# Kernel optimization log

Measured on AMD Instinct MI355X. Metric: run time of the kernel, lower is better.

Reference implementation:

```python
import jax, jax.numpy as jnp
import numpy as np

N, D, H, L = 100000, 128, 4, 2
C = D // H  # per-head channels
E = 1600000
NEG_SLOPE = 0.2
LN_EPS = 1e-5


def setup_inputs() -> dict:
    key = jax.random.key(0)
    ks = jax.random.split(key, 8)
    x = jax.random.normal(ks[0], (N, D), dtype=jnp.float32)
    edge_index = jax.random.randint(ks[1], (2, E), 0, N, dtype=jnp.int64)
    s = 1.0 / np.sqrt(D)
    Wl = jax.random.normal(ks[2], (L, D, D), dtype=jnp.float32) * s
    Wr = jax.random.normal(ks[3], (L, D, D), dtype=jnp.float32) * s
    att = jax.random.normal(ks[4], (L, H, C), dtype=jnp.float32) * (1.0 / np.sqrt(C))
    bias = jnp.zeros((L, D), dtype=jnp.float32)
    gamma = jnp.ones((L, D), dtype=jnp.float32)
    beta = jnp.zeros((L, D), dtype=jnp.float32)
    return {"x": x, "edge_index": edge_index, "Wl": Wl, "Wr": Wr,
            "att": att, "bias": bias, "gamma": gamma, "beta": beta}


def _gatv2_layer(h, src, dst, Wl, Wr, att, bias):
    # h: (N, D); src/dst: (E2,) with self-loops already appended
    xl = (h @ Wl).reshape(N, H, C)  # source-side transform
    xr = (h @ Wr).reshape(N, H, C)  # target-side transform
    e = jax.nn.leaky_relu(xl[src] + xr[dst], NEG_SLOPE)      # (E2, H, C)
    alpha = jnp.einsum('ehc,hc->eh', e, att)                 # (E2, H)
    # segment softmax over incoming edges of each destination node
    m = jax.ops.segment_max(alpha, dst, num_segments=N)      # (N, H)
    ea = jnp.exp(alpha - m[dst])
    s = jax.ops.segment_sum(ea, dst, num_segments=N)         # (N, H)
    a = ea / s[dst]                                          # (E2, H)
    out = jax.ops.segment_sum(a[:, :, None] * xl[src], dst, num_segments=N)
    return out.reshape(N, D) + bias


def _layer_norm(y, gamma, beta):
    mu = jnp.mean(y, axis=-1, keepdims=True)
    var = jnp.var(y, axis=-1, keepdims=True)
    return (y - mu) * jax.lax.rsqrt(var + LN_EPS) * gamma + beta


def reference(x, edge_index, Wl, Wr, att, bias, gamma, beta):
    # PyG GATv2Conv defaults: add_self_loops=True (eval mode: dropouts identity)
    loops = jnp.arange(N, dtype=edge_index.dtype)
    src = jnp.concatenate([edge_index[0], loops])
    dst = jnp.concatenate([edge_index[1], loops])
    h = x
    for l in range(L):
        g = _gatv2_layer(h, src, dst, Wl[l], Wr[l], att[l], bias[l])
        h = h + jax.nn.elu(_layer_norm(g, gamma[l], beta[l]))
    return h
```

## Files before the change

kernel.cpp:

```cpp
#include <hip/hip_runtime.h>
#include <hip/hip_fp16.h>
#include <math.h>

#define N_NODES 100000
#define D_FEAT  128
#define E_EDGES 1600000
#define E2      (E_EDGES + N_NODES)
#define NEG_SLOPE 0.2f
#define LN_EPS    1e-5f

#define NB   391
#define TS   8192
#define NTIL ((E2 + TS - 1) / TS)
#define PREPB 65

typedef __attribute__((ext_vector_type(4))) float floatx4;
typedef _Float16 h2 __attribute__((ext_vector_type(2)));
typedef _Float16 h8 __attribute__((ext_vector_type(8)));

static __device__ __forceinline__ float fdot2f(h2 a, h2 b, float c) {
#if __has_builtin(__builtin_amdgcn_fdot2)
    return __builtin_amdgcn_fdot2(a, b, c, false);
#else
    return (float)a[0] * (float)b[0] + (float)a[1] * (float)b[1] + c;
#endif
}

static __device__ __forceinline__ h2 shfl_xor_h2(h2 v, int off) {
    int i = __builtin_bit_cast(int, v);
    i = __shfl_xor(i, off);
    return __builtin_bit_cast(h2, i);
}

__global__ __launch_bounds__(1024) void tile_count_prep(
        const int* __restrict__ edge_dst,
        const float* __restrict__ Wl, const float* __restrict__ Wr,
        const float* __restrict__ att,
        _Float16* __restrict__ Wt, _Float16* __restrict__ atth,
        int* __restrict__ bcnt, int* __restrict__ toff,
        unsigned short* __restrict__ rankbuf) {
    const int b = blockIdx.x;
    const int t = threadIdx.x;
    if (b >= NTIL) {
        int gid = (b - NTIL) * 1024 + t;
        if (gid < 65536) {
            int l = gid >> 15, rem = gid & 32767, side = rem >> 14, cw = rem & 16383;
            int col = cw >> 7, k = cw & 127;
            const float* W = side ? Wr : Wl;
            Wt[gid] = (_Float16)W[l * 16384 + k * 128 + col];
        } else if (gid < 65536 + 256) {
            atth[gid - 65536] = (_Float16)att[gid - 65536];
        }
        return;
    }
    __shared__ int h[NB];
    if (t < NB) h[t] = 0;
    __syncthreads();
    const int base = b * TS;
#pragma unroll
    for (int j = 0; j < TS / 1024; ++j) {
        int i = base + j * 1024 + t;
        if (i < E2) {
            int d = (i < E_EDGES) ? edge_dst[i] : (i - E_EDGES);
            int rk = atomicAdd(&h[d >> 8], 1);
            rankbuf[i] = (unsigned short)rk;
        }
    }
    __syncthreads();
    if (t < NB) toff[b * NB + t] = atomicAdd(&bcnt[t], h[t]);
}

__global__ __launch_bounds__(512) void bucket_scan(const int* __restrict__ bcnt,
                                                   int* __restrict__ bstart,
                                                   int* __restrict__ rowstart) {
    __shared__ int s[512];
    const int t = threadIdx.x;
    int v = (t < NB) ? bcnt[t] : 0;
    s[t] = v;
    __syncthreads();
    for (int off = 1; off < 512; off <<= 1) {
        int x = (t >= off) ? s[t - off] : 0;
        __syncthreads();
        s[t] += x;
        __syncthreads();
    }
    if (t <= NB) bstart[t] = s[t] - v;
    if (t == 0) rowstart[N_NODES] = E2;
}

__global__ __launch_bounds__(1024) void tile_scatter(const int* __restrict__ edge_src,
                                                     const int* __restrict__ edge_dst,
                                                     const int* __restrict__ bstart,
                                                     const int* __restrict__ toff,
                                                     const unsigned short* __restrict__ rankbuf,
                                                     unsigned* __restrict__ pairbuf) {
    __shared__ int base[NB];
    const int t = threadIdx.x;
    if (t < NB) base[t] = bstart[t] + toff[blockIdx.x * NB + t];
    __syncthreads();
    const int tb = blockIdx.x * TS;
#pragma unroll
    for (int j = 0; j < TS / 1024; ++j) {
        int i = tb + j * 1024 + t;
        if (i < E2) {
            int d, sr;
            if (i < E_EDGES) { d = edge_dst[i]; sr = edge_src[i]; }
            else             { d = i - E_EDGES; sr = d; }
            int b = d >> 8;
            int pos = base[b] + (int)rankbuf[i];
            pairbuf[pos] = (unsigned)sr | ((unsigned)(d & 255) << 17);
        }
    }
}

__global__ __launch_bounds__(1024) void bucketize(const unsigned* __restrict__ pairbuf,
                                                  const int* __restrict__ bstart,
                                                  int* __restrict__ rowstart,
                                                  int* __restrict__ csr_src) {
    __shared__ int cnt[256], off[256];
    const int blk = blockIdx.x;
    const int t = threadIdx.x;
    const int nbase = blk << 8;
    if (t < 256) cnt[t] = 0;
    __syncthreads();
    const int e0 = bstart[blk], e1 = bstart[blk + 1];

    unsigned pr0, pr1, pr2, pr3, pr4, pr5, pr6, pr7;
    int rk0, rk1, rk2, rk3, rk4, rk5, rk6, rk7;
#define LOADP(K, PR)  { int p = e0 + t + (K) * 1024; PR = (p < e1) ? pairbuf[p] : 0u; }
    LOADP(0, pr0) LOADP(1, pr1) LOADP(2, pr2) LOADP(3, pr3)
    LOADP(4, pr4) LOADP(5, pr5) LOADP(6, pr6) LOADP(7, pr7)
#undef LOADP
#define HIST(K, PR, RK) { int p = e0 + t + (K) * 1024; \
        RK = (p < e1) ? atomicAdd(&cnt[PR >> 17], 1) : 0; }
    HIST(0, pr0, rk0) HIST(1, pr1, rk1) HIST(2, pr2, rk2) HIST(3, pr3, rk3)
    HIST(4, pr4, rk4) HIST(5, pr5, rk5) HIST(6, pr6, rk6) HIST(7, pr7, rk7)
#undef HIST
    __syncthreads();

    int v = (t < 256) ? cnt[t] : 0;
    __shared__ int sc[256];
    if (t < 256) sc[t] = v;
    __syncthreads();
    for (int o = 1; o < 256; o <<= 1) {
        int x = (t < 256 && t >= o) ? sc[t - o] : 0;
        __syncthreads();
        if (t < 256) sc[t] += x;
        __syncthreads();
    }
    if (t < 256) {
        int excl = sc[t] - v;
        int node = nbase + t;
        if (node < N_NODES) rowstart[node] = e0 + excl;
        off[t] = e0 + excl;
    }
    __syncthreads();

#define SCAT(K, PR, RK) { int p = e0 + t + (K) * 1024; \
        if (p < e1) csr_src[off[PR >> 17] + RK] = (int)(PR & 0x1FFFF); }
    SCAT(0, pr0, rk0) SCAT(1, pr1, rk1) SCAT(2, pr2, rk2) SCAT(3, pr3, rk3)
    SCAT(4, pr4, rk4) SCAT(5, pr5, rk5) SCAT(6, pr6, rk6) SCAT(7, pr7, rk7)
#undef SCAT
}

__global__ __launch_bounds__(256) void gemm_mfma5(
        const _Float16* __restrict__ hA,
        const float* __restrict__ Afp,
        const _Float16* __restrict__ Wt,
        _Float16* __restrict__ xl, _Float16* __restrict__ xr, int n_rows) {
    __shared__ char bsm[65536];
    const int tid  = threadIdx.x;
    const int wave = tid >> 6;
    const int lane = tid & 63;
    const int m = lane & 15;
    const int q = lane >> 4;
    const int r0 = (blockIdx.x * 4 + wave) * 32;

#pragma unroll
    for (int k = 0; k < 16; ++k) {
        int ci  = tid + k * 256;
        int row = ci >> 4;
        int off = (ci & 15) << 4;
        uint4 v = *(const uint4*)((const char*)Wt + row * 256 + off);
        *(uint4*)(bsm + row * 256 + (off ^ ((row & 7) << 4))) = v;
    }
    __syncthreads();

    int arow0 = r0 + m;        if (arow0 >= n_rows) arow0 = n_rows - 1;
    int arow1 = r0 + 16 + m;   if (arow1 >= n_rows) arow1 = n_rows - 1;

    floatx4 acc[2][2][8];
#pragma unroll
    for (int s = 0; s < 2; ++s)
#pragma unroll
        for (int rt = 0; rt < 2; ++rt)
#pragma unroll
            for (int ct = 0; ct < 8; ++ct) acc[s][rt][ct] = (floatx4){0.f,0.f,0.f,0.f};

    const int swz = (m & 7) << 4;
#pragma unroll
    for (int ks = 0; ks < 4; ++ks) {
        const int k0 = ks * 32 + q * 8;
        const int cb = k0 * 2;
        h8 a0, a1;
        if (Afp) {
            float4 f0 = *(const float4*)(Afp + (size_t)arow0 * 128 + k0);
            float4 f1 = *(const float4*)(Afp + (size_t)arow0 * 128 + k0 + 4);
            float4 g0 = *(const float4*)(Afp + (size_t)arow1 * 128 + k0);
            float4 g1 = *(const float4*)(Afp + (size_t)arow1 * 128 + k0 + 4);
            a0 = (h8){(_Float16)f0.x, (_Float16)f0.y, (_Float16)f0.z, (_Float16)f0.w,
                      (_Float16)f1.x, (_Float16)f1.y, (_Float16)f1.z, (_Float16)f1.w};
            a1 = (h8){(_Float16)g0.x, (_Float16)g0.y, (_Float16)g0.z, (_Float16)g0.w,
                      (_Float16)g1.x, (_Float16)g1.y, (_Float16)g1.z, (_Float16)g1.w};
        } else {
            a0 = *(const h8*)(hA + (size_t)arow0 * 128 + k0);
            a1 = *(const h8*)(hA + (size_t)arow1 * 128 + k0);
        }
#pragma unroll
        for (int s = 0; s < 2; ++s) {
#pragma unroll
            for (int ct = 0; ct < 8; ++ct) {
                int row = s * 128 + ct * 16 + m;
                h8 bfrag = *(const h8*)(bsm + row * 256 + (cb ^ swz));
                acc[s][0][ct] = __builtin_amdgcn_mfma_f32_16x16x32_f16(a0, bfrag, acc[s][0][ct], 0, 0, 0);
                acc[s][1][ct] = __builtin_amdgcn_mfma_f32_16x16x32_f16(a1, bfrag, acc[s][1][ct], 0, 0, 0);
            }
        }
    }

#pragma unroll
    for (int s = 0; s < 2; ++s) {
        _Float16* out = s ? xr : xl;
#pragma unroll
        for (int rt = 0; rt < 2; ++rt)
#pragma unroll
            for (int ct = 0; ct < 8; ++ct)
#pragma unroll
                for (int i = 0; i < 4; ++i) {
                    int row = r0 + rt * 16 + q * 4 + i;
                    if (row < n_rows)
                        out[(size_t)row * 128 + ct * 16 + m] = (_Float16)acc[s][rt][ct][i];
                }
    }
}

union U16 { uint4 u; h2 h[4]; };

__global__ __launch_bounds__(256) void gat_node10(
        const _Float16* __restrict__ xl,
        const _Float16* __restrict__ xr,
        const float* __restrict__ h_in_f32,
        const _Float16* __restrict__ h_in_f16,
        const int* __restrict__ rowstart, const int* __restrict__ csr_src,
        const _Float16* __restrict__ atth, const float* __restrict__ bias,
        const float* __restrict__ gamma, const float* __restrict__ beta,
        float* __restrict__ out_f32,
        _Float16* __restrict__ out_f16) {
    const int wave = threadIdx.x >> 6;
    const int lane = threadIdx.x & 63;
    const int node = blockIdx.x * 4 + wave;
    const int esub = lane >> 3;
    const int r    = lane & 7;
    const int c0   = r * 16;
    const int c    = c0 + 2 * esub;

    const int p0 = rowstart[node], p1 = rowstart[node + 1];
    const int pe = p1 - 1;

    U16 xra, xrb, ata, atb;
    {
        const uint4* xp = (const uint4*)(xr + (size_t)node * 128 + c0);
        xra.u = xp[0]; xrb.u = xp[1];
        const uint4* ap = (const uint4*)(atth + c0);
        ata.u = ap[0]; atb.u = ap[1];
    }
    const float2 bi = *(const float2*)(bias + c);
    const h2 ns2 = {(_Float16)NEG_SLOPE, (_Float16)NEG_SLOPE};

    const unsigned short* xls = (const unsigned short*)xl;

    float s = 0.f;
    h2 acc2[8];
#pragma unroll
    for (int j = 0; j < 8; ++j) acc2[j] = (h2){(_Float16)0.f, (_Float16)0.f};

    auto consume = [&](const U16& u0, const U16& u1, bool v) {
        float da = 0.f, db = 0.f;
#pragma unroll
        for (int qq = 0; qq < 4; ++qq) {
            h2 z  = u0.h[qq] + xra.h[qq];
            h2 lk = __builtin_elementwise_max(z, z * ns2);
            da = fdot2f(lk, ata.h[qq], da);
        }
#pragma unroll
        for (int qq = 0; qq < 4; ++qq) {
            h2 z  = u1.h[qq] + xrb.h[qq];
            h2 lk = __builtin_elementwise_max(z, z * ns2);
            db = fdot2f(lk, atb.h[qq], db);
        }
        float d = da + db;
        float alpha = d + __shfl_xor(d, 1);
        float w = v ? __expf(alpha) : 0.f;
        s += w;
        h2 w2 = {(_Float16)w, (_Float16)w};
#pragma unroll
        for (int qq = 0; qq < 4; ++qq)
            acc2[qq] = w2 * u0.h[qq] + acc2[qq];
#pragma unroll
        for (int qq = 0; qq < 4; ++qq)
            acc2[qq + 4] = w2 * u1.h[qq] + acc2[qq + 4];
    };

    int pA = p0 + esub;        if (pA > pe) pA = pe;
    int pB = p0 + 8 + esub;    if (pB > pe) pB = pe;
    int pC = p0 + 16 + esub;   if (pC > pe) pC = pe;
    int i0 = csr_src[pA];
    int i1 = csr_src[pB];
    int i2 = csr_src[pC];

    U16 s0a, s0b, s1a, s1b, s2a, s2b;
    { const uint4* rp = (const uint4*)(xls + (size_t)i0 * 128 + c0); s0a.u = rp[0]; s0b.u = rp[1]; }
    { const uint4* rp = (const uint4*)(xls + (size_t)i1 * 128 + c0); s1a.u = rp[0]; s1b.u = rp[1]; }

    int pb = p0;
    for (;;) {
        {
            int pn = pb + 24 + esub; if (pn > pe) pn = pe;
            int inew = csr_src[pn];
            if (pb + 16 < p1) {
                const uint4* rp = (const uint4*)(xls + (size_t)i2 * 128 + c0);
                s2a.u = rp[0]; s2b.u = rp[1];
            }
            consume(s0a, s0b, (pb + esub) < p1);
            i0 = inew;
            pb += 8; if (pb >= p1) break;
        }
        {
            int pn = pb + 24 + esub; if (pn > pe) pn = pe;
            int inew = csr_src[pn];
            if (pb + 16 < p1) {
                const uint4* rp = (const uint4*)(xls + (size_t)i0 * 128 + c0);
                s0a.u = rp[0]; s0b.u = rp[1];
            }
            consume(s1a, s1b, (pb + esub) < p1);
            i1 = inew;
            pb += 8; if (pb >= p1) break;
        }
        {
            int pn = pb + 24 + esub; if (pn > pe) pn = pe;
            int inew = csr_src[pn];
            if (pb + 16 < p1) {
                const uint4* rp = (const uint4*)(xls + (size_t)i1 * 128 + c0);
                s1a.u = rp[0]; s1b.u = rp[1];
            }
            consume(s2a, s2b, (pb + esub) < p1);
            i2 = inew;
            pb += 8; if (pb >= p1) break;
        }
    }

    float ssum = s;
    ssum += __shfl_xor(ssum, 8);
    ssum += __shfl_xor(ssum, 16);
    ssum += __shfl_xor(ssum, 32);

    const bool sel0 = (esub & 1) != 0;
    const bool sel1 = ((esub >> 1) & 1) != 0;
    const bool sel2 = ((esub >> 2) & 1) != 0;
    h2 b4[4];
#pragma unroll
    for (int k = 0; k < 4; ++k) {
        h2 keep = sel0 ? acc2[2 * k + 1] : acc2[2 * k];
        h2 send = sel0 ? acc2[2 * k]     : acc2[2 * k + 1];
        b4[k] = keep + shfl_xor_h2(send, 8);
    }
    h2 c2[2];
#pragma unroll
    for (int k = 0; k < 2; ++k) {
        h2 keep = sel1 ? b4[2 * k + 1] : b4[2 * k];
        h2 send = sel1 ? b4[2 * k]     : b4[2 * k + 1];
        c2[k] = keep + shfl_xor_h2(send, 16);
    }
    h2 keepf = sel2 ? c2[1] : c2[0];
    h2 sendf = sel2 ? c2[0] : c2[1];
    h2 tot = keepf + shfl_xor_h2(sendf, 32);

    const float invS = 1.f / ssum;
    float g0 = (float)tot[0] * invS + bi.x;
    float g1 = (float)tot[1] * invS + bi.y;

    const float2 ga = *(const float2*)(gamma + c);
    const float2 be = *(const float2*)(beta + c);
    float hx, hy;
    if (h_in_f16) {
        h2 hv = *(const h2*)(h_in_f16 + (size_t)node * 128 + c);
        hx = (float)hv[0]; hy = (float)hv[1];
    } else {
        float2 hv = *(const float2*)(h_in_f32 + (size_t)node * 128 + c);
        hx = hv.x; hy = hv.y;
    }

    float sum = g0 + g1, sq = g0 * g0 + g1 * g1;
#pragma unroll
    for (int off = 1; off < 64; off <<= 1) {
        sum += __shfl_xor(sum, off);
        sq  += __shfl_xor(sq, off);
    }
    float mu   = sum * (1.f / 128.f);
    float var  = sq * (1.f / 128.f) - mu * mu;
    float rstd = rsqrtf(var + LN_EPS);
    float y0 = (g0 - mu) * rstd * ga.x + be.x;
    float y1 = (g1 - mu) * rstd * ga.y + be.y;
    float e0 = (y0 > 0.f) ? y0 : (__expf(y0) - 1.f);
    float e1 = (y1 > 0.f) ? y1 : (__expf(y1) - 1.f);

    float ox = hx + e0;
    float oy = hy + e1;
    if (out_f32) {
        float2 o; o.x = ox; o.y = oy;
        *(float2*)(out_f32 + (size_t)node * 128 + c) = o;
    } else {
        h2 po = {(_Float16)ox, (_Float16)oy};
        *(h2*)(out_f16 + (size_t)node * 128 + c) = po;
    }
}

extern "C" void kernel_launch(void* const* d_in, const int* in_sizes, int n_in,
                              void* d_out, int out_size, void* d_ws, size_t ws_size,
                              hipStream_t stream) {
    const float* x     = (const float*)d_in[0];
    const int*   eidx  = (const int*)d_in[1];
    const float* Wl    = (const float*)d_in[2];
    const float* Wr    = (const float*)d_in[3];
    const float* att   = (const float*)d_in[4];
    const float* bias  = (const float*)d_in[5];
    const float* gamma = (const float*)d_in[6];
    const float* beta  = (const float*)d_in[7];
    float* out = (float*)d_out;

    char* ws = (char*)d_ws;
    _Float16* xl = (_Float16*)ws;              ws += (size_t)N_NODES * 128 * 2;
    _Float16* xr = (_Float16*)ws;              ws += (size_t)N_NODES * 128 * 2;
    _Float16* h16 = (_Float16*)ws;             ws += (size_t)N_NODES * 128 * 2;
    _Float16* Wt  = (_Float16*)ws;             ws += (size_t)65536 * 2;
    _Float16* atth = (_Float16*)ws;            ws += 256 * 2;
    unsigned* pairbuf = (unsigned*)ws;         ws += (size_t)E2 * 4;
    unsigned short* rankbuf = (unsigned short*)ws; ws += (size_t)E2 * 2;
    int* toff     = (int*)ws; ws += (size_t)NTIL * NB * 4;
    int* bcnt     = (int*)ws; ws += (NB + 1) * 4;
    int* bstart   = (int*)ws; ws += (NB + 1) * 4;
    int* rowstart = (int*)ws; ws += (size_t)(N_NODES + 4) * 4;
    int* csr_src  = (int*)ws; ws += (size_t)E2 * 4;

    const int* edge_src = eidx;
    const int* edge_dst = eidx + E_EDGES;

    hipMemsetAsync(bcnt, 0, (NB + 1) * sizeof(int), stream);
    tile_count_prep<<<NTIL + PREPB, 1024, 0, stream>>>(
        edge_dst, Wl, Wr, att, Wt, atth, bcnt, toff, rankbuf);
    bucket_scan<<<1, 512, 0, stream>>>(bcnt, bstart, rowstart);
    tile_scatter<<<NTIL, 1024, 0, stream>>>(edge_src, edge_dst, bstart, toff,
                                            rankbuf, pairbuf);
    bucketize<<<NB, 1024, 0, stream>>>(pairbuf, bstart, rowstart, csr_src);

    const int gemm_gx = (N_NODES + 127) / 128;
    for (int l = 0; l < 2; ++l) {
        gemm_mfma5<<<gemm_gx, 256, 0, stream>>>(
            (l == 0) ? nullptr : h16, (l == 0) ? x : nullptr,
            Wt + (size_t)l * 32768, xl, xr, N_NODES);
        gat_node10<<<N_NODES / 4, 256, 0, stream>>>(
            xl, xr,
            (l == 0) ? x : nullptr, (l == 0) ? nullptr : h16,
            rowstart, csr_src,
            atth + l * 128, bias + l * 128, gamma + l * 128, beta + l * 128,
            (l == 1) ? out : nullptr, (l == 0) ? h16 : nullptr);
    }
}
```

Before: 357.0 us.

## Fuse edge bucket count and scatter using fixed-capacity bucket slots

Merges tile counting, global scan and tile scatter into one kernel by giving each destination bucket a fixed-capacity region (MAXB slots) in pairbuf. A block's offset now comes straight from the atomic on the bucket count, so the separate scan kernel, the rankbuf round trip and the toff buffer are gone. The per-bucket global prefix is recomputed inside each bucketize block. This removes two kernel launches and extra global traffic. The risk is overflow if any bucket gets more than 8192 edges, which holds for uniform random inputs but not in general, and edges inside a bucket now land in nondeterministic order.

```diff
diff --git a/kernel.cpp b/kernel.cpp
--- a/kernel.cpp
+++ b/kernel.cpp
@@ -13,6 +13,7 @@
 #define TS   8192
 #define NTIL ((E2 + TS - 1) / TS)
 #define PREPB 65
+#define MAXB 8192
 
 typedef __attribute__((ext_vector_type(4))) float floatx4;
 typedef _Float16 h2 __attribute__((ext_vector_type(2)));
@@ -32,13 +33,12 @@
     return __builtin_bit_cast(h2, i);
 }
 
-__global__ __launch_bounds__(1024) void tile_count_prep(
-        const int* __restrict__ edge_dst,
+__global__ __launch_bounds__(1024) void count_scatter_prep(
+        const int* __restrict__ edge_src, const int* __restrict__ edge_dst,
         const float* __restrict__ Wl, const float* __restrict__ Wr,
         const float* __restrict__ att,
         _Float16* __restrict__ Wt, _Float16* __restrict__ atth,
-        int* __restrict__ bcnt, int* __restrict__ toff,
-        unsigned short* __restrict__ rankbuf) {
+        int* __restrict__ bcnt, unsigned* __restrict__ pairbuf) {
     const int b = blockIdx.x;
     const int t = threadIdx.x;
     if (b >= NTIL) {
@@ -54,110 +54,93 @@
         return;
     }
     __shared__ int h[NB];
+    __shared__ int base[NB];
     if (t < NB) h[t] = 0;
     __syncthreads();
-    const int base = b * TS;
-#pragma unroll
-    for (int j = 0; j < TS / 1024; ++j) {
-        int i = base + j * 1024 + t;
+    const int tb = b * TS;
+    int pk[8];
+#pragma unroll
+    for (int j = 0; j < 8; ++j) {
+        int i = tb + j * 1024 + t;
+        int d = 0, rk = 0;
         if (i < E2) {
-            int d = (i < E_EDGES) ? edge_dst[i] : (i - E_EDGES);
-            int rk = atomicAdd(&h[d >> 8], 1);
-            rankbuf[i] = (unsigned short)rk;
-        }
-    }
-    __syncthreads();
-    if (t < NB) toff[b * NB + t] = atomicAdd(&bcnt[t], h[t]);
-}
-
-__global__ __launch_bounds__(512) void bucket_scan(const int* __restrict__ bcnt,
-                                                   int* __restrict__ bstart,
-                                                   int* __restrict__ rowstart) {
-    __shared__ int s[512];
-    const int t = threadIdx.x;
-    int v = (t < NB) ? bcnt[t] : 0;
-    s[t] = v;
-    __syncthreads();
-    for (int off = 1; off < 512; off <<= 1) {
-        int x = (t >= off) ? s[t - off] : 0;
-        __syncthreads();
-        s[t] += x;
-        __syncthreads();
-    }
-    if (t <= NB) bstart[t] = s[t] - v;
-    if (t == 0) rowstart[N_NODES] = E2;
-}
-
-__global__ __launch_bounds__(1024) void tile_scatter(const int* __restrict__ edge_src,
-                                                     const int* __restrict__ edge_dst,
-                                                     const int* __restrict__ bstart,
-                                                     const int* __restrict__ toff,
-                                                     const unsigned short* __restrict__ rankbuf,
-                                                     unsigned* __restrict__ pairbuf) {
-    __shared__ int base[NB];
-    const int t = threadIdx.x;
-    if (t < NB) base[t] = bstart[t] + toff[blockIdx.x * NB + t];
-    __syncthreads();
-    const int tb = blockIdx.x * TS;
-#pragma unroll
-    for (int j = 0; j < TS / 1024; ++j) {
+            d = (i < E_EDGES) ? edge_dst[i] : (i - E_EDGES);
+            rk = atomicAdd(&h[d >> 8], 1);
+        }
+        pk[j] = d | (rk << 17);
+    }
+    __syncthreads();
+    if (t < NB) base[t] = t * MAXB + atomicAdd(&bcnt[t], h[t]);
+    __syncthreads();
+#pragma unroll
+    for (int j = 0; j < 8; ++j) {
         int i = tb + j * 1024 + t;
         if (i < E2) {
-            int d, sr;
-            if (i < E_EDGES) { d = edge_dst[i]; sr = edge_src[i]; }
-            else             { d = i - E_EDGES; sr = d; }
-            int b = d >> 8;
-            int pos = base[b] + (int)rankbuf[i];
-            pairbuf[pos] = (unsigned)sr | ((unsigned)(d & 255) << 17);
-        }
-    }
-}
-
-__global__ __launch_bounds__(1024) void bucketize(const unsigned* __restrict__ pairbuf,
-                                                  const int* __restrict__ bstart,
-                                                  int* __restrict__ rowstart,
-                                                  int* __restrict__ csr_src) {
+            int d  = pk[j] & 0x1FFFF;
+            int rk = pk[j] >> 17;
+            int sr = (i < E_EDGES) ? edge_src[i] : d;
+            pairbuf[base[d >> 8] + rk] =
+                (unsigned)sr | ((unsigned)(d & 255) << 17);
+        }
+    }
+}
+
+__global__ __launch_bounds__(1024) void bucketize2(
+        const unsigned* __restrict__ pairbuf, const int* __restrict__ bcnt,
+        int* __restrict__ rowstart, int* __restrict__ csr_src) {
+    __shared__ int s[512];
     __shared__ int cnt[256], off[256];
     const int blk = blockIdx.x;
     const int t = threadIdx.x;
+
+    if (t < 512) s[t] = (t < NB) ? bcnt[t] : 0;
+    __syncthreads();
+    for (int o = 1; o < 512; o <<= 1) {
+        int x = (t < 512 && t >= o) ? s[t - o] : 0;
+        __syncthreads();
+        if (t < 512) s[t] += x;
+        __syncthreads();
+    }
+    const int count = bcnt[blk];
+    const int g0 = s[blk] - count;
+    const int e0 = blk * MAXB;
     const int nbase = blk << 8;
     if (t < 256) cnt[t] = 0;
     __syncthreads();
-    const int e0 = bstart[blk], e1 = bstart[blk + 1];
 
     unsigned pr0, pr1, pr2, pr3, pr4, pr5, pr6, pr7;
     int rk0, rk1, rk2, rk3, rk4, rk5, rk6, rk7;
-#define LOADP(K, PR)  { int p = e0 + t + (K) * 1024; PR = (p < e1) ? pairbuf[p] : 0u; }
+#define LOADP(K, PR)  { int p = t + (K) * 1024; PR = (p < count) ? pairbuf[e0 + p] : 0u; }
     LOADP(0, pr0) LOADP(1, pr1) LOADP(2, pr2) LOADP(3, pr3)
     LOADP(4, pr4) LOADP(5, pr5) LOADP(6, pr6) LOADP(7, pr7)
 #undef LOADP
-#define HIST(K, PR, RK) { int p = e0 + t + (K) * 1024; \
-        RK = (p < e1) ? atomicAdd(&cnt[PR >> 17], 1) : 0; }
+#define HIST(K, PR, RK) { int p = t + (K) * 1024; \
+        RK = (p < count) ? atomicAdd(&cnt[PR >> 17], 1) : 0; }
     HIST(0, pr0, rk0) HIST(1, pr1, rk1) HIST(2, pr2, rk2) HIST(3, pr3, rk3)
     HIST(4, pr4, rk4) HIST(5, pr5, rk5) HIST(6, pr6, rk6) HIST(7, pr7, rk7)
 #undef HIST
     __syncthreads();
 
     int v = (t < 256) ? cnt[t] : 0;
-    __shared__ int sc[256];
-    if (t < 256) sc[t] = v;
+    if (t < 256) s[t] = v;
     __syncthreads();
     for (int o = 1; o < 256; o <<= 1) {
-        int x = (t < 256 && t >= o) ? sc[t - o] : 0;
+        int x = (t < 256 && t >= o) ? s[t - o] : 0;
         __syncthreads();
-        if (t < 256) sc[t] += x;
+        if (t < 256) s[t] += x;
         __syncthreads();
     }
     if (t < 256) {
-        int excl = sc[t] - v;
+        int excl = s[t] - v;
         int node = nbase + t;
-        if (node < N_NODES) rowstart[node] = e0 + excl;
-        off[t] = e0 + excl;
-    }
-    __syncthreads();
-
-#define SCAT(K, PR, RK) { int p = e0 + t + (K) * 1024; \
-        if (p < e1) csr_src[off[PR >> 17] + RK] = (int)(PR & 0x1FFFF); }
+        if (node < N_NODES) rowstart[node] = g0 + excl;
+        off[t] = g0 + excl;
+    }
+    if (blk == 0 && t == 0) rowstart[N_NODES] = E2;
+    __syncthreads();
+
+#define SCAT(K, PR, RK) { int p = t + (K) * 1024; \
+        if (p < count) csr_src[off[PR >> 17] + RK] = (int)(PR & 0x1FFFF); }
     SCAT(0, pr0, rk0) SCAT(1, pr1, rk1) SCAT(2, pr2, rk2) SCAT(3, pr3, rk3)
     SCAT(4, pr4, rk4) SCAT(5, pr5, rk5) SCAT(6, pr6, rk6) SCAT(7, pr7, rk7)
 #undef SCAT
@@ -444,11 +427,8 @@
     _Float16* h16 = (_Float16*)ws;             ws += (size_t)N_NODES * 128 * 2;
     _Float16* Wt  = (_Float16*)ws;             ws += (size_t)65536 * 2;
     _Float16* atth = (_Float16*)ws;            ws += 256 * 2;
-    unsigned* pairbuf = (unsigned*)ws;         ws += (size_t)E2 * 4;
-    unsigned short* rankbuf = (unsigned short*)ws; ws += (size_t)E2 * 2;
-    int* toff     = (int*)ws; ws += (size_t)NTIL * NB * 4;
+    unsigned* pairbuf = (unsigned*)ws;         ws += (size_t)NB * MAXB * 4;
     int* bcnt     = (int*)ws; ws += (NB + 1) * 4;
-    int* bstart   = (int*)ws; ws += (NB + 1) * 4;
     int* rowstart = (int*)ws; ws += (size_t)(N_NODES + 4) * 4;
     int* csr_src  = (int*)ws; ws += (size_t)E2 * 4;
 
@@ -456,12 +436,9 @@
     const int* edge_dst = eidx + E_EDGES;
 
     hipMemsetAsync(bcnt, 0, (NB + 1) * sizeof(int), stream);
-    tile_count_prep<<<NTIL + PREPB, 1024, 0, stream>>>(
-        edge_dst, Wl, Wr, att, Wt, atth, bcnt, toff, rankbuf);
-    bucket_scan<<<1, 512, 0, stream>>>(bcnt, bstart, rowstart);
-    tile_scatter<<<NTIL, 1024, 0, stream>>>(edge_src, edge_dst, bstart, toff,
-                                            rankbuf, pairbuf);
-    bucketize<<<NB, 1024, 0, stream>>>(pairbuf, bstart, rowstart, csr_src);
+    count_scatter_prep<<<NTIL + PREPB, 1024, 0, stream>>>(
+        edge_src, edge_dst, Wl, Wr, att, Wt, atth, bcnt, pairbuf);
+    bucketize2<<<NB, 1024, 0, stream>>>(pairbuf, bcnt, rowstart, csr_src);
 
     const int gemm_gx = (N_NODES + 127) / 128;
     for (int l = 0; l < 2; ++l) {
```

Result: no change. 356.5 us (-0.1%).
